# Performance work log

Measured on AMD Instinct MI355X. Metric: run time of the kernel, lower is better.

The kernel has to match this reference:

```python
import jax, jax.numpy as jnp
import numpy as np

B, N, M, K = 2, 4096, 512, 50
EMB, OUT = 512, 128
EPS = 1e-5


def _sqdist(a, b):
    # a: [B,P,D], b: [B,Q,D] -> squared euclidean distances [B,P,Q]
    return (jnp.sum(a * a, -1)[:, :, None] + jnp.sum(b * b, -1)[:, None, :]
            - 2.0 * jnp.einsum('bpd,bqd->bpq', a, b))


def _graph_feature(x, xg, k):
    # x: [B,D,N] points, xg: [B,D,M] grid -> edge features [B,2D,N,k]
    xt = x.transpose(0, 2, 1)   # [B,N,D]
    gt = xg.transpose(0, 2, 1)  # [B,M,D]
    nearest = jnp.argmin(_sqdist(xt, gt), axis=-1)               # [B,N] nearest grid pt per point
    _, nbr = jax.lax.top_k(-_sqdist(gt, gt), k)                  # [B,M,k] kNN within grid
    idx = jnp.take_along_axis(nbr, nearest[:, :, None], axis=1)  # [B,N,k]
    b = x.shape[0]
    feat = gt[jnp.arange(b)[:, None, None], idx]                 # [B,N,k,D] gathered grid feats
    feat = feat.at[:, :, 0, :].set(xt)                           # slot 0 <- point's own feature
    ctr = xt[:, :, None, :]
    out = jnp.concatenate([feat - ctr, jnp.broadcast_to(ctr, feat.shape)], axis=-1)
    return out.transpose(0, 3, 1, 2)                             # [B,2D,N,k]


def _lrelu(x):
    return jnp.where(x >= 0, x, 0.2 * x)


def _bn(y, g, bt, axes):
    # BatchNorm forward with batch statistics (torch training-mode math, biased var)
    m = jnp.mean(y, axis=axes, keepdims=True)
    v = jnp.mean((y - m) ** 2, axis=axes, keepdims=True)
    sh = [1] * y.ndim
    sh[1] = -1
    return (y - m) / jnp.sqrt(v + EPS) * g.reshape(sh) + bt.reshape(sh)


def _conv2(x, W, g, bt):
    # 1x1 Conv2d (no bias) + BN2d + LeakyReLU(0.2)
    return _lrelu(_bn(jnp.einsum('oc,bcnk->bonk', W, x), g, bt, (0, 2, 3)))


def _conv1(x, W, g, bt):
    # 1x1 Conv1d (no bias) + BN1d + LeakyReLU(0.2)
    return _lrelu(_bn(jnp.einsum('oc,bcn->bon', W, x), g, bt, (0, 2)))


def _forward(x, x_grid, FPS, W1, W2, W3, W4, W5, W6, W7, W8, W9,
             g1, g2, g3, g4, g5, g6, g7, g8,
             b1, b2, b3, b4, b5, b6, b7, b8):
    f = _graph_feature(x, x_grid, K)
    f = _conv2(f, W1, g1, b1)
    f = _conv2(f, W2, g2, b2)
    x1 = f.max(-1)                                               # [B,64,N]
    x1g = jnp.take_along_axis(x1, FPS[:, None, :], axis=2)       # [B,64,M]
    f = _graph_feature(x1, x1g, K)
    f = _conv2(f, W3, g3, b3)
    f = _conv2(f, W4, g4, b4)
    x2 = f.max(-1)
    x2g = jnp.take_along_axis(x2, FPS[:, None, :], axis=2)
    f = _graph_feature(x2, x2g, K)
    f = _conv2(f, W5, g5, b5)
    x3 = f.max(-1)
    x3g = jnp.take_along_axis(x3, FPS[:, None, :], axis=2)
    xg = jnp.concatenate([x1g, x2g, x3g], axis=1)                # [B,192,M]
    xg = _conv1(xg, W6, g6, b6)                                  # [B,EMB,M]
    xg = jnp.broadcast_to(xg.max(-1, keepdims=True), (x.shape[0], EMB, x.shape[2]))
    h = jnp.concatenate([xg, x1, x2, x3], axis=1)                # [B,EMB+192,N]
    h = _conv1(h, W7, g7, b7)
    h = _conv1(h, W8, g8, b8)
    h = jnp.einsum('oc,bcn->bon', W9, h)                         # final conv9, no BN/act
    return h.transpose(0, 2, 1)                                  # [B,N,OUT]


def setup_inputs() -> dict:
    key = jax.random.key(0)
    ks = jax.random.split(key, 32)
    def w(i, o, c):
        return jax.random.normal(ks[i], (o, c), jnp.float32) * 0.1
    inp = {
        'x': jax.random.normal(ks[0], (B, 3, N), jnp.float32),
        'x_grid': jax.random.normal(ks[1], (B, 3, M), jnp.float32),
        'FPS': jax.random.randint(ks[2], (B, M), 0, N),
        'W1': w(3, 64, 6), 'W2': w(4, 64, 64), 'W3': w(5, 64, 128),
        'W4': w(6, 64, 64), 'W5': w(7, 64, 128), 'W6': w(8, EMB, 192),
        'W7': w(9, 128, 192 + EMB), 'W8': w(10, 64, 128), 'W9': w(11, OUT, 64),
    }
    dims = [64, 64, 64, 64, 64, EMB, 128, 64]
    for j, d in enumerate(dims):
        inp[f'g{j+1}'] = 1.0 + 0.05 * jax.random.normal(ks[12 + j], (d,), jnp.float32)
        inp[f'b{j+1}'] = 0.05 * jax.random.normal(ks[20 + j], (d,), jnp.float32)
    return inp


def reference(x, x_grid, FPS, W1, W2, W3, W4, W5, W6, W7, W8, W9,
              g1, g2, g3, g4, g5, g6, g7, g8,
              b1, b2, b3, b4, b5, b6, b7, b8):
    return _forward(x, x_grid, FPS, W1, W2, W3, W4, W5, W6, W7, W8, W9,
                    g1, g2, g3, g4, g5, g6, g7, g8,
                    b1, b2, b3, b4, b5, b6, b7, b8)
```

## Files before the change

### kernel.cpp

```cpp
#include <hip/hip_runtime.h>
#include <hip/hip_bf16.h>

#define DEV __device__ __forceinline__
using bf16 = __hip_bfloat16;
using u16 = unsigned short;
using u64 = unsigned long long;

static constexpr int B_ = 2, N_ = 4096, M_ = 512, K_ = 50;
static constexpr int BN = B_ * N_;
static constexpr int BM = B_ * M_;
static constexpr float EPS_ = 1e-5f;

DEV float lrelu(float z) { return z < 0.f ? 0.2f * z : z; }
DEV int clampi(int v, int hi) { return ((unsigned)v < (unsigned)hi) ? v : 0; }

DEV u16 f2bfu(float f) {
    unsigned u = __float_as_uint(f);
    return (u16)((u + 0x7fffu + ((u >> 16) & 1u)) >> 16);
}
DEV float bfu2f(u16 h) { return __uint_as_float((unsigned)h << 16); }

typedef short bf8v __attribute__((ext_vector_type(8)));
typedef float f4v __attribute__((ext_vector_type(4)));

__global__ void k_detect(const unsigned short* __restrict__ xw, int* __restrict__ flag) {
    int t = threadIdx.x;
    int cnt = 0;
    for (int i = t; i < 4096; i += 256) {
        int e = (xw[i] >> 7) & 0xFF;
        if (e >= 100 && e <= 140) cnt++;
    }
    __shared__ int sh[256];
    sh[t] = cnt;
    __syncthreads();
    for (int s = 128; s; s >>= 1) { if (t < s) sh[t] += sh[t + s]; __syncthreads(); }
    if (t == 0) *flag = (sh[0] >= 3300) ? 1 : 0;
}

struct CvtDesc { const void* src; float* dst; int n; };
struct CvtArgs { CvtDesc d[25]; };
__global__ void k_convert(CvtArgs a, const int* __restrict__ flag) {
    CvtDesc dd = a.d[blockIdx.y];
    int i = blockIdx.x * 256 + threadIdx.x;
    if (i >= dd.n) return;
    float v = (*flag) ? __bfloat162float(((const bf16*)dd.src)[i])
                      : ((const float*)dd.src)[i];
    dd.dst[i] = v;
}

struct CvtT { const void* src; float* dst; int O; int C; int stride; int off; };
struct CvtTArgs { CvtT d[6]; };
__global__ void k_convT(CvtTArgs a, const int* __restrict__ flag) {
    CvtT dd = a.d[blockIdx.y];
    int idx = blockIdx.x * 256 + threadIdx.x;
    if (idx >= dd.O * dd.C) return;
    int c = idx / dd.O, o = idx % dd.O;
    int si = o * dd.stride + dd.off + c;
    float v = (*flag) ? __bfloat162float(((const bf16*)dd.src)[si])
                      : ((const float*)dd.src)[si];
    dd.dst[idx] = v;
}

__global__ void k_wfrag(const float* __restrict__ Wa, const float* __restrict__ Wb,
                        u16* __restrict__ fa, u16* __restrict__ fb) {
    const float* W = blockIdx.y ? Wb : Wa;
    u16* f = blockIdx.y ? fb : fa;
    int t = blockIdx.x * 256 + threadIdx.x;
    int j = t & 7, l = (t >> 3) & 63, s = (t >> 9) & 1, n = (t >> 10) & 3;
    int o = n * 16 + (l & 15);
    int c = s * 32 + (l >> 4) * 8 + j;
    float v = W[o * 64 + c];
    u16 hi = f2bfu(v);
    u16 lo = f2bfu(v - bfu2f(hi));
    f[t] = hi;
    f[4096 + t] = lo;
}

__global__ void k_ubuf(const float* __restrict__ Pg, const float* __restrict__ prm,
                       float* __restrict__ ub) {
    int t = blockIdx.x * 256 + threadIdx.x;
    int c = t & 63;
    ub[t] = fmaf(prm[c], Pg[t], prm[64 + c]);
}

DEV float rdval(const void* p, int i, int isbf) {
    return isbf ? __bfloat162float(((const bf16*)p)[i]) : ((const float*)p)[i];
}
__global__ void k_transpose(const void* __restrict__ x, const void* __restrict__ xg,
                            const int* __restrict__ flag,
                            float* __restrict__ xt, float* __restrict__ gt,
                            float* __restrict__ gT3, float* __restrict__ gn) {
    int isbf = *flag;
    int idx = blockIdx.x * 256 + threadIdx.x;
    if (idx < BN * 3) {
        int c = idx / BN, i = idx % BN;
        int b = i / N_, n = i % N_;
        xt[i * 3 + c] = rdval(x, (b * 3 + c) * N_ + n, isbf);
    } else {
        int r = idx - BN * 3;
        if (r < BM) {
            int b = r / M_, m = r % M_;
            float s = 0.f;
            for (int c = 0; c < 3; c++) {
                float v = rdval(xg, (b * 3 + c) * M_ + m, isbf);
                gt[r * 3 + c] = v;
                gT3[(b * 3 + c) * M_ + m] = v;
                s = fmaf(v, v, s);
            }
            gn[r] = s;
        }
    }
}

DEV void nearest3_body(int blk, const float* __restrict__ q, const float* __restrict__ gt,
                       const float* __restrict__ gn, int* __restrict__ nearest) {
    int sub = threadIdx.x & 15;
    int pt = blk * 16 + (threadIdx.x >> 4);
    int b = pt >> 12;
    float q0 = q[pt * 3], q1 = q[pt * 3 + 1], q2 = q[pt * 3 + 2];
    float qn = q0 * q0 + q1 * q1 + q2 * q2;
    const float* gb = gt + (size_t)b * M_ * 3;
    const float* gnb = gn + b * M_;
    float best = 1e30f; int bi = 0x7fffffff;
    for (int j = 0; j < 32; j++) {
        int m = sub + 16 * j;
        float dot = q0 * gb[m * 3] + q1 * gb[m * 3 + 1] + q2 * gb[m * 3 + 2];
        float dv = qn + gnb[m] - 2.f * dot;
        if (dv < best || (dv == best && m < bi)) { best = dv; bi = m; }
    }
    for (int off = 8; off; off >>= 1) {
        float ov = __shfl_xor(best, off);
        int oi = __shfl_xor(bi, off);
        if (ov < best || (ov == best && oi < bi)) { best = ov; bi = oi; }
    }
    if (sub == 0) nearest[pt] = clampi(bi, M_);
}

DEV void nearest64_body_v4(int blk, const float* __restrict__ q,
                           const float* __restrict__ gT, const float* __restrict__ gn,
                           int* __restrict__ nearest,
                           float (*__restrict__ lg)[512], float (*__restrict__ ql)[64]) {
    int lane = threadIdx.x & 63;
    int tid = threadIdx.x;
    int w = __builtin_amdgcn_readfirstlane(threadIdx.x >> 6);
    int pt0 = blk * 16 + w * 4;
    int b = pt0 >> 12;
    const float* gTb = gT + (size_t)b * 64 * M_;
    {
        const float4* q4 = (const float4*)(q + (size_t)(blk * 16) * 64);
        ((float4*)ql)[tid] = q4[tid];
    }
    float qn[4] = {0.f, 0.f, 0.f, 0.f};
    float d[4][8] = {};
#pragma clang loop unroll(disable)
    for (int ch = 0; ch < 8; ch++) {
        __syncthreads();
        {
            const float4* src = (const float4*)(gTb + (size_t)ch * 8 * M_);
            float4* dst = (float4*)lg;
#pragma unroll
            for (int i = 0; i < 4; i++) {
                int idx = i * 256 + tid;
                dst[idx] = src[idx];
            }
        }
        __syncthreads();
#pragma unroll
        for (int j = 0; j < 8; j++) {
            float4 g0 = *(const float4*)&lg[j][4 * lane];
            float4 g1 = *(const float4*)&lg[j][256 + 4 * lane];
#pragma unroll
            for (int p = 0; p < 4; p++) {
                float qc = ql[w * 4 + p][ch * 8 + j];
                qn[p] = fmaf(qc, qc, qn[p]);
                d[p][0] = fmaf(qc, g0.x, d[p][0]); d[p][1] = fmaf(qc, g0.y, d[p][1]);
                d[p][2] = fmaf(qc, g0.z, d[p][2]); d[p][3] = fmaf(qc, g0.w, d[p][3]);
                d[p][4] = fmaf(qc, g1.x, d[p][4]); d[p][5] = fmaf(qc, g1.y, d[p][5]);
                d[p][6] = fmaf(qc, g1.z, d[p][6]); d[p][7] = fmaf(qc, g1.w, d[p][7]);
            }
        }
    }
    const float* gnb = gn + b * M_;
    float4 n0 = *(const float4*)(gnb + 4 * lane);
    float4 n1 = *(const float4*)(gnb + 256 + 4 * lane);
    float nn[8] = {n0.x, n0.y, n0.z, n0.w, n1.x, n1.y, n1.z, n1.w};
#pragma clang loop unroll(disable)
    for (int p = 0; p < 4; p++) {
        float best = 1e30f; int bi = 0;
#pragma unroll
        for (int i = 0; i < 8; i++) {
            int m = (i < 4) ? (4 * lane + i) : (256 + 4 * lane + i - 4);
            float dv = qn[p] + nn[i] - 2.f * d[p][i];
            if (dv < best || (dv == best && m < bi)) { best = dv; bi = m; }
        }
        for (int off = 32; off; off >>= 1) {
            float ov = __shfl_xor(best, off);
            int oi = __shfl_xor(bi, off);
            if (ov < best || (ov == best && oi < bi)) { best = ov; bi = oi; }
        }
        if (lane == 0) nearest[pt0 + p] = clampi(bi, M_);
    }
}

DEV void select50(const float dd[8], const int mreg[8], int lane,
                  int* __restrict__ rowp, int* __restrict__ idxrow) {
    u64 key[8];
#pragma unroll
    for (int i = 0; i < 8; i++) {
        unsigned u = __float_as_uint(dd[i]);
        if (u == 0x80000000u) u = 0u;
        u = (u & 0x80000000u) ? ~u : (u | 0x80000000u);
        key[i] = ((u64)u << 9) | (u64)(unsigned)mreg[i];
    }
    u64 kmin = key[0];
#pragma unroll
    for (int i = 1; i < 8; i++) kmin = key[i] < kmin ? key[i] : kmin;
    for (int off = 32; off; off >>= 1) {
        u64 o = __shfl_xor(kmin, off);
        kmin = o < kmin ? o : kmin;
    }
    u64 res = 0;
#pragma clang loop unroll(disable)
    for (int bit = 40; bit >= 0; --bit) {
        u64 t = res | ((u64)1 << bit);
        int c = 0;
#pragma unroll
        for (int i = 0; i < 8; i++) c += (key[i] < t) ? 1 : 0;
        u64 b0 = __ballot(c & 1), b1 = __ballot(c & 2), b2 = __ballot(c & 4), b3 = __ballot(c & 8);
        int tot = __popcll(b0) + 2 * __popcll(b1) + 4 * __popcll(b2) + 8 * __popcll(b3);
        if (tot <= K_ - 1) res = t;
    }
    int lc = 0, loc[8];
    bool sel[8];
#pragma unroll
    for (int i = 0; i < 8; i++) {
        sel[i] = (key[i] <= res) && (key[i] != kmin);
        loc[i] = lc;
        lc += sel[i] ? 1 : 0;
    }
    u64 lmask = ((u64)1 << lane) - 1;
    u64 c0 = __ballot(lc & 1), c1 = __ballot(lc & 2), c2 = __ballot(lc & 4), c3 = __ballot(lc & 8);
    int pre = __popcll(c0 & lmask) + 2 * __popcll(c1 & lmask)
            + 4 * __popcll(c2 & lmask) + 8 * __popcll(c3 & lmask);
#pragma unroll
    for (int i = 0; i < 8; i++) {
        if (key[i] == kmin) { rowp[0] = mreg[i]; idxrow[0] = mreg[i]; }
        if (sel[i]) { int p = 1 + pre + loc[i]; rowp[p] = mreg[i]; idxrow[p] = mreg[i]; }
    }
}

DEV void nbr3_body(int blk, const float* __restrict__ g, const float* __restrict__ gT,
                   const float* __restrict__ gn, const float* __restrict__ Pg,
                   int* __restrict__ nbr, float* __restrict__ T1, float* __restrict__ T2,
                   float* __restrict__ Mn, float* __restrict__ Mx,
                   int (*__restrict__ idxb)[64]) {
    int lane = threadIdx.x & 63, w = threadIdx.x >> 6;
    int row = blk * 4 + w;
    int b = row >> 9;
    const float* grow = g + (size_t)row * 3;
    float qn = gn[row];
    const float* gTb = gT + (size_t)b * 3 * M_;
    const float* gnb = gn + b * M_;
    float d[8] = {0.f, 0.f, 0.f, 0.f, 0.f, 0.f, 0.f, 0.f};
    {
        float qs[3];
#pragma unroll
        for (int c = 0; c < 3; c++) qs[c] = grow[c];
#pragma unroll
        for (int c = 0; c < 3; c++) {
            float qc = qs[c];
            float4 g0 = *(const float4*)(gTb + c * M_ + 4 * lane);
            float4 g1 = *(const float4*)(gTb + c * M_ + 256 + 4 * lane);
            d[0] = fmaf(qc, g0.x, d[0]); d[1] = fmaf(qc, g0.y, d[1]);
            d[2] = fmaf(qc, g0.z, d[2]); d[3] = fmaf(qc, g0.w, d[3]);
            d[4] = fmaf(qc, g1.x, d[4]); d[5] = fmaf(qc, g1.y, d[5]);
            d[6] = fmaf(qc, g1.z, d[6]); d[7] = fmaf(qc, g1.w, d[7]);
        }
    }
    float4 n0 = *(const float4*)(gnb + 4 * lane);
    float4 n1 = *(const float4*)(gnb + 256 + 4 * lane);
    float dd[8];
    dd[0] = qn + n0.x - 2.f * d[0]; dd[1] = qn + n0.y - 2.f * d[1];
    dd[2] = qn + n0.z - 2.f * d[2]; dd[3] = qn + n0.w - 2.f * d[3];
    dd[4] = qn + n1.x - 2.f * d[4]; dd[5] = qn + n1.y - 2.f * d[5];
    dd[6] = qn + n1.z - 2.f * d[6]; dd[7] = qn + n1.w - 2.f * d[7];
    int mreg[8];
#pragma unroll
    for (int i = 0; i < 8; i++) mreg[i] = (i < 4) ? (4 * lane + i) : (256 + 4 * lane + i - 4);
    select50(dd, mreg, lane, nbr + (size_t)row * K_, idxb[w]);
    int myIdx = idxb[w][lane];
    const float* Pgb = Pg + (size_t)b * M_ * 64;
    float t1 = 0.f, t2 = 0.f, mn = 1e30f, mx = -1e30f;
#pragma unroll 7
    for (int k = 1; k < K_; k++) {
        int idx = clampi(__shfl(myIdx, k), M_);
        float v = Pgb[(size_t)idx * 64 + lane];
        t1 += v; t2 = fmaf(v, v, t2);
        mn = fminf(mn, v); mx = fmaxf(mx, v);
    }
    size_t o = (size_t)row * 64 + lane;
    T1[o] = t1; T2[o] = t2; Mn[o] = mn; Mx[o] = mx;
}

DEV void nbr64_body(int blk, const float* __restrict__ g, const float* __restrict__ gT,
                    const float* __restrict__ gn, const float* __restrict__ Pg,
                    int* __restrict__ nbr, float* __restrict__ T1, float* __restrict__ T2,
                    float* __restrict__ Mn, float* __restrict__ Mx,
                    float (*__restrict__ lg)[512], float (*__restrict__ ql)[64],
                    int (*__restrict__ idxb)[64]) {
    int lane = threadIdx.x & 63, w = threadIdx.x >> 6;
    int tid = threadIdx.x;
    int row = blk * 4 + w;
    int b = row >> 9;
    float qn = gn[row];
    const float* gTb = gT + (size_t)b * 64 * M_;
    const float* gnb = gn + b * M_;
    if (tid < 64) {
        const float4* q4 = (const float4*)(g + (size_t)(blk * 4) * 64);
        ((float4*)ql)[tid] = q4[tid];
    }
    float d[8] = {0.f, 0.f, 0.f, 0.f, 0.f, 0.f, 0.f, 0.f};
#pragma clang loop unroll(disable)
    for (int ch = 0; ch < 8; ch++) {
        __syncthreads();
        {
            const float4* src = (const float4*)(gTb + (size_t)ch * 8 * M_);
            float4* dst = (float4*)lg;
#pragma unroll
            for (int i = 0; i < 4; i++) {
                int idx = i * 256 + tid;
                dst[idx] = src[idx];
            }
        }
        __syncthreads();
#pragma unroll
        for (int j = 0; j < 8; j++) {
            float qc = ql[w][ch * 8 + j];
            float4 g0 = *(const float4*)&lg[j][4 * lane];
            float4 g1 = *(const float4*)&lg[j][256 + 4 * lane];
            d[0] = fmaf(qc, g0.x, d[0]); d[1] = fmaf(qc, g0.y, d[1]);
            d[2] = fmaf(qc, g0.z, d[2]); d[3] = fmaf(qc, g0.w, d[3]);
            d[4] = fmaf(qc, g1.x, d[4]); d[5] = fmaf(qc, g1.y, d[5]);
            d[6] = fmaf(qc, g1.z, d[6]); d[7] = fmaf(qc, g1.w, d[7]);
        }
    }
    float4 n0 = *(const float4*)(gnb + 4 * lane);
    float4 n1 = *(const float4*)(gnb + 256 + 4 * lane);
    float dd[8];
    dd[0] = qn + n0.x - 2.f * d[0]; dd[1] = qn + n0.y - 2.f * d[1];
    dd[2] = qn + n0.z - 2.f * d[2]; dd[3] = qn + n0.w - 2.f * d[3];
    dd[4] = qn + n1.x - 2.f * d[4]; dd[5] = qn + n1.y - 2.f * d[5];
    dd[6] = qn + n1.z - 2.f * d[6]; dd[7] = qn + n1.w - 2.f * d[7];
    int mreg[8];
#pragma unroll
    for (int i = 0; i < 8; i++) mreg[i] = (i < 4) ? (4 * lane + i) : (256 + 4 * lane + i - 4);
    select50(dd, mreg, lane, nbr + (size_t)row * K_, idxb[w]);
    int myIdx = idxb[w][lane];
    const float* Pgb = Pg + (size_t)b * M_ * 64;
    float t1 = 0.f, t2 = 0.f, mn = 1e30f, mx = -1e30f;
#pragma unroll 7
    for (int k = 1; k < K_; k++) {
        int idx = clampi(__shfl(myIdx, k), M_);
        float v = Pgb[(size_t)idx * 64 + lane];
        t1 += v; t2 = fmaf(v, v, t2);
        mn = fminf(mn, v); mx = fmaxf(mx, v);
    }
    size_t o = (size_t)row * 64 + lane;
    T1[o] = t1; T2[o] = t2; Mn[o] = mn; Mx[o] = mx;
}

__global__ __launch_bounds__(256) void k_knn3(
    const float* __restrict__ q, const float* __restrict__ gt, const float* __restrict__ gT3,
    const float* __restrict__ gn, const float* __restrict__ Pg,
    int* __restrict__ nearest, int* __restrict__ nbr, float* __restrict__ T1,
    float* __restrict__ T2, float* __restrict__ Mn, float* __restrict__ Mx) {
    __shared__ int idxb[4][64];
    if (blockIdx.x < BN / 16) nearest3_body(blockIdx.x, q, gt, gn, nearest);
    else nbr3_body(blockIdx.x - BN / 16, gt, gT3, gn, Pg, nbr, T1, T2, Mn, Mx, idxb);
}
__global__ __launch_bounds__(256) void k_knn64(
    const float* __restrict__ q, const float* __restrict__ xgt, const float* __restrict__ gT,
    const float* __restrict__ gn, const float* __restrict__ Pg,
    int* __restrict__ nearest, int* __restrict__ nbr, float* __restrict__ T1,
    float* __restrict__ T2, float* __restrict__ Mn, float* __restrict__ Mx) {
    __shared__ float lg[8][512];
    __shared__ float ql[16][64];
    __shared__ int idxb[4][64];
    if (blockIdx.x < BN / 16) nearest64_body_v4(blockIdx.x, q, gT, gn, nearest, lg, ql);
    else nbr64_body(blockIdx.x - BN / 16, xgt, gT, gn, Pg, nbr, T1, T2, Mn, Mx, lg, ql, idxb);
}

#define STATS_STORE_64(s1v, s2v, partial)                                         \
    {                                                                             \
        __shared__ float r1_[256], r2_[256];                                      \
        r1_[threadIdx.x] = (s1v); r2_[threadIdx.x] = (s2v);                       \
        __syncthreads();                                                          \
        if (threadIdx.x < 64) {                                                   \
            int t_ = threadIdx.x;                                                 \
            float a1_ = r1_[t_] + r1_[t_ + 64] + r1_[t_ + 128] + r1_[t_ + 192];   \
            float a2_ = r2_[t_] + r2_[t_ + 64] + r2_[t_ + 128] + r2_[t_ + 192];   \
            float* sp_ = (partial) + (size_t)blockIdx.x * 128;                    \
            sp_[t_] = a1_; sp_[64 + t_] = a2_;                                    \
        }                                                                         \
    }

__global__ __launch_bounds__(256) void k_pgrid3(const float* __restrict__ g,
                                                const float* __restrict__ W1,
                                                float* __restrict__ Pg) {
    int lane = threadIdx.x & 63;
    int row = blockIdx.x * 4 + __builtin_amdgcn_readfirstlane(threadIdx.x >> 6);
    float c0 = g[row * 3], c1 = g[row * 3 + 1], c2 = g[row * 3 + 2];
    const float* wr = W1 + lane * 6;
    Pg[(size_t)row * 64 + lane] = fmaf(wr[0], c0, fmaf(wr[1], c1, wr[2] * c2));
}

__global__ __launch_bounds__(256) void k_gridprep(
    const float* __restrict__ xsrc, const int* __restrict__ FPS,
    const float* __restrict__ Wt, float* __restrict__ xgt, float* __restrict__ gT,
    float* __restrict__ gn, float* __restrict__ Pg) {
    int lane = threadIdx.x & 63, w = threadIdx.x >> 6;
    int row = blockIdx.x * 4 + w;
    int b = row >> 9, m = row & 511;
    int src = b * N_ + clampi(FPS[row], N_);
    float ge = xsrc[(size_t)src * 64 + lane];
    xgt[(size_t)row * 64 + lane] = ge;
    gT[((size_t)b * 64 + lane) * M_ + m] = ge;
    float s = 0.f, acc = 0.f;
#pragma unroll
    for (int c = 0; c < 64; c++) {
        float vc = __shfl(ge, c);
        s = fmaf(vc, vc, s);
        acc = fmaf(Wt[c * 64 + lane], vc, acc);
    }
    Pg[(size_t)row * 64 + lane] = acc;
    if (lane == 0) gn[row] = s;
}

template <int D>
__global__ __launch_bounds__(256) void k_prep_stats(
    const float* __restrict__ q, const float* __restrict__ W1,
    const int* __restrict__ nearest, const float* __restrict__ T1,
    const float* __restrict__ T2, float* __restrict__ D0, float* __restrict__ S0,
    float* __restrict__ partial) {
    int lane = threadIdx.x & 63;
    int pt = blockIdx.x * 4 + __builtin_amdgcn_readfirstlane(threadIdx.x >> 6);
    int b = pt >> 12;
    float pa, pb;
    if constexpr (D == 3) {
        float c0 = q[pt * 3], c1 = q[pt * 3 + 1], c2 = q[pt * 3 + 2];
        const float* wr = W1 + lane * 6;
        pa = fmaf(wr[0], c0, fmaf(wr[1], c1, wr[2] * c2));
        pb = fmaf(wr[3], c0, fmaf(wr[4], c1, wr[5] * c2));
    } else {
        float ge = q[(size_t)pt * 64 + lane];
        pa = 0.f; pb = 0.f;
#pragma unroll
        for (int c = 0; c < 64; c++) {
            float sh = __shfl(ge, c);
            pa = fmaf(W1[c * 64 + lane], sh, pa);
            pb = fmaf(W1[(64 + c) * 64 + lane], sh, pb);
        }
    }
    float d0 = pb - pa, s0 = pb;
    size_t t = (size_t)pt * 64 + lane;
    D0[t] = d0;
    S0[t] = s0;
    size_t nr = ((size_t)b * M_ + clampi(nearest[pt], M_)) * 64 + lane;
    float t1 = T1[nr], t2 = T2[nr];
    float s1 = s0 + fmaf(49.f, d0, t1);
    float s2 = fmaf(s0, s0, fmaf(49.f * d0, d0, fmaf(2.f * d0, t1, t2)));
    STATS_STORE_64(s1, s2, partial)
}

__global__ void k_apply0(const float* __restrict__ D0, const float* __restrict__ S0,
                         const int* __restrict__ nearest, const float* __restrict__ Mn,
                         const float* __restrict__ Mx, const float* __restrict__ prm,
                         float* __restrict__ xout) {
    int t = blockIdx.x * 256 + threadIdx.x;
    int pt = t >> 6, o = t & 63;
    int b = pt >> 12;
    size_t nr = ((size_t)b * M_ + clampi(nearest[pt], M_)) * 64 + o;
    float d0 = D0[t], s0 = S0[t];
    float a = prm[o], sh = prm[64 + o];
    float v = a > 0.f ? fmaxf(s0, d0 + Mx[nr]) : fminf(s0, d0 + Mn[nr]);
    xout[t] = lrelu(fmaf(a, v, sh));
}

__global__ __launch_bounds__(256) void k_pass1_mfma(
    const float* __restrict__ ub, const float* __restrict__ D0,
    const float* __restrict__ S0, const int* __restrict__ nearest,
    const int* __restrict__ nbr, const float* __restrict__ prm1,
    const u16* __restrict__ wf, const float* __restrict__ zero64,
    float* __restrict__ partial,
    float* __restrict__ mn_out, float* __restrict__ mx_out) {
    __shared__ u16 Zs[2][2][4096];
    float* ls1 = (float*)&Zs[0][0][0];
    float* ls2 = ls1 + 128;
    int l = threadIdx.x & 63;
    int w = threadIdx.x >> 6;
    int wp = w >> 1, nh = w & 1;
    bf8v whi[2][2], wlo[2][2];
#pragma unroll
    for (int nt = 0; nt < 2; nt++)
#pragma unroll
        for (int s = 0; s < 2; s++) {
            int fi = (((nh * 2 + nt) * 2 + s) * 64 + l) * 8;
            whi[nt][s] = *(const bf8v*)(wf + fi);
            wlo[nt][s] = *(const bf8v*)(wf + 4096 + fi);
        }
    {
        int tt = threadIdx.x & 127;
        int p = threadIdx.x >> 7;
        int k = tt & 63, ch = tt >> 6;
        int pt = blockIdx.x * 2 + p, b = pt >> 12;
        int nr = clampi(nearest[pt], M_);
        const int* nrow = nbr + ((size_t)b * M_ + nr) * K_;
        int idx = (k >= 1 && k < K_) ? clampi(nrow[k], M_) : 0;
        const float4* src = ((k == 0) ? (const float4*)(S0 + (size_t)pt * 64)
                                      : (const float4*)(ub + ((size_t)b * M_ + idx) * 64)) + ch * 8;
        const float4* d4 = ((k == 0) ? (const float4*)zero64
                                     : (const float4*)(D0 + (size_t)pt * 64)) + ch * 8;
        const float4* a4 = (const float4*)(prm1) + ch * 8;
        const float4* s4 = (const float4*)(prm1 + 64) + ch * 8;
        bool pad = (k >= K_);
        char* zh = (char*)&Zs[p][0][0];
        char* zl = (char*)&Zs[p][1][0];
        int swz = (k & 7) << 4;
#pragma unroll
        for (int q2 = 0; q2 < 4; q2++) {
            unsigned hv[4], lv[4];
#pragma unroll
            for (int h = 0; h < 2; h++) {
                float4 u = src[q2 * 2 + h], d = d4[q2 * 2 + h];
                float4 a = a4[q2 * 2 + h];
                if (k == 0) {
                    float4 s = s4[q2 * 2 + h];
                    u.x = fmaf(a.x, u.x, s.x); u.y = fmaf(a.y, u.y, s.y);
                    u.z = fmaf(a.z, u.z, s.z); u.w = fmaf(a.w, u.w, s.w);
                }
                float z0 = lrelu(fmaf(a.x, d.x, u.x));
                float z1 = lrelu(fmaf(a.y, d.y, u.y));
                float z2 = lrelu(fmaf(a.z, d.z, u.z));
                float z3 = lrelu(fmaf(a.w, d.w, u.w));
                if (pad) { z0 = 0.f; z1 = 0.f; z2 = 0.f; z3 = 0.f; }
                unsigned h0 = f2bfu(z0), h1 = f2bfu(z1), h2 = f2bfu(z2), h3 = f2bfu(z3);
                unsigned l0 = __float_as_uint(z0 - bfu2f((u16)h0)) >> 16;
                unsigned l1 = __float_as_uint(z1 - bfu2f((u16)h1)) >> 16;
                unsigned l2 = __float_as_uint(z2 - bfu2f((u16)h2)) >> 16;
                unsigned l3 = __float_as_uint(z3 - bfu2f((u16)h3)) >> 16;
                hv[h * 2] = h0 | (h1 << 16); hv[h * 2 + 1] = h2 | (h3 << 16);
                lv[h * 2] = l0 | (l1 << 16); lv[h * 2 + 1] = l2 | (l3 << 16);
            }
            int ad = k * 128 + ((ch * 64 + q2 * 16) ^ swz);
            *(uint4*)(zh + ad) = make_uint4(hv[0], hv[1], hv[2], hv[3]);
            *(uint4*)(zl + ad) = make_uint4(lv[0], lv[1], lv[2], lv[3]);
        }
    }
    __syncthreads();
    int pt = blockIdx.x * 2 + wp;
    const char* zh = (const char*)&Zs[wp][0][0];
    const char* zl = (const char*)&Zs[wp][1][0];
    f4v acc[4][2] = {};
#pragma unroll
    for (int s = 0; s < 2; s++) {
        bf8v ah[4], al[4];
#pragma unroll
        for (int m = 0; m < 4; m++) {
            int row = m * 16 + (l & 15);
            int ad = row * 128 + (((s * 64) + ((l >> 4) * 16)) ^ ((row & 7) << 4));
            ah[m] = *(const bf8v*)(zh + ad);
            al[m] = *(const bf8v*)(zl + ad);
        }
#pragma unroll
        for (int m = 0; m < 4; m++)
#pragma unroll
            for (int nt = 0; nt < 2; nt++) {
                acc[m][nt] = __builtin_amdgcn_mfma_f32_16x16x32_bf16(ah[m], whi[nt][s], acc[m][nt], 0, 0, 0);
                acc[m][nt] = __builtin_amdgcn_mfma_f32_16x16x32_bf16(al[m], whi[nt][s], acc[m][nt], 0, 0, 0);
                acc[m][nt] = __builtin_amdgcn_mfma_f32_16x16x32_bf16(ah[m], wlo[nt][s], acc[m][nt], 0, 0, 0);
            }
    }
    __syncthreads();
    int rg = (l >> 4) * 4;
#pragma unroll
    for (int nt = 0; nt < 2; nt++) {
        float s1 = 0.f, s2 = 0.f, mn = 1e30f, mx = -1e30f;
#pragma unroll
        for (int m = 0; m < 4; m++)
#pragma unroll
            for (int i = 0; i < 4; i++) {
                int kk = m * 16 + rg + i;
                float v = acc[m][nt][i];
                if (kk < K_) { s1 += v; s2 = fmaf(v, v, s2); mn = fminf(mn, v); mx = fmaxf(mx, v); }
            }
        for (int off = 16; off <= 32; off <<= 1) {
            s1 += __shfl_xor(s1, off); s2 += __shfl_xor(s2, off);
            mn = fminf(mn, __shfl_xor(mn, off)); mx = fmaxf(mx, __shfl_xor(mx, off));
        }
        if (l < 16) {
            int o = nh * 32 + nt * 16 + l;
            mn_out[(size_t)pt * 64 + o] = mn;
            mx_out[(size_t)pt * 64 + o] = mx;
            ls1[wp * 64 + o] = s1;
            ls2[wp * 64 + o] = s2;
        }
    }
    __syncthreads();
    if (threadIdx.x < 64) {
        int t = threadIdx.x;
        float* sp = partial + (size_t)blockIdx.x * 128;
        sp[t] = ls1[t] + ls1[64 + t];
        sp[64 + t] = ls2[t] + ls2[64 + t];
    }
}

__global__ void k_apply(const float* __restrict__ mn, const float* __restrict__ mx,
                        const float* __restrict__ prm, float* __restrict__ xout) {
    int t = blockIdx.x * 256 + threadIdx.x;
    int o = t & 63;
    float a = prm[o], sh = prm[64 + o];
    float v = a > 0.f ? mx[t] : mn[t];
    xout[t] = lrelu(fmaf(a, v, sh));
}

template <int NP, int O>
__global__ __launch_bounds__(256) void k_redfin(
    const float* __restrict__ partial, double* __restrict__ red,
    int* __restrict__ counter, int C,
    const float* __restrict__ g, const float* __restrict__ bt,
    float* __restrict__ prm) {
    constexpr int VALS = 2 * O;
    constexpr int G = NP / 32;
    int b = blockIdx.x;
    for (int v = threadIdx.x; v < VALS; v += 256) {
        const float* p = partial + (size_t)b * G * VALS + v;
        double s = 0.0;
#pragma unroll
        for (int k = 0; k < G; k++) s += p[(size_t)k * VALS];
        red[(size_t)b * VALS + v] = s;
    }
    __threadfence();
    __syncthreads();
    __shared__ bool isLast;
    if (threadIdx.x == 0) isLast = (atomicAdd(counter, 1) == 31);
    __syncthreads();
    if (!isLast) return;
    __threadfence();
    for (int o = threadIdx.x; o < O; o += 256) {
        double s1 = 0.0, s2 = 0.0;
#pragma unroll
        for (int k = 0; k < 32; k++) {
            s1 += red[(size_t)k * VALS + o];
            s2 += red[(size_t)k * VALS + O + o];
        }
        double m = s1 / C, var = s2 / C - m * m;
        if (var < 0) var = 0;
        float sc = g[o] / sqrtf((float)var + EPS_);
        prm[o] = sc;
        prm[O + o] = bt[o] - (float)m * sc;
    }
}

__global__ __launch_bounds__(256) void k_conv_w6(
    const float* __restrict__ x1gt, const float* __restrict__ x2gt,
    const float* __restrict__ x3t, const int* __restrict__ FPS,
    const float* __restrict__ W6t, float* __restrict__ y6, float* __restrict__ partial) {
    __shared__ float vl[4][192];
    int b = blockIdx.x / 128;
    int m0 = (blockIdx.x % 128) * 4;
    for (int i = threadIdx.x; i < 4 * 192; i += 256) {
        int mi = i / 192, c = i % 192;
        float v;
        if (c < 128) {
            const float* src = c < 64 ? x1gt : x2gt;
            v = src[((size_t)b * M_ + m0 + mi) * 64 + (c & 63)];
        } else {
            int s = b * N_ + clampi(FPS[b * M_ + m0 + mi], N_);
            v = x3t[(size_t)s * 64 + (c - 128)];
        }
        vl[mi][c] = v;
    }
    __syncthreads();
    float acc0[4] = {0}, acc1[4] = {0};
    int o0 = threadIdx.x, o1 = threadIdx.x + 256;
    for (int c = 0; c < 192; c++) {
        float w0 = W6t[c * 512 + o0];
        float w1 = W6t[c * 512 + o1];
#pragma unroll
        for (int m = 0; m < 4; m++) { float v = vl[m][c]; acc0[m] = fmaf(w0, v, acc0[m]); acc1[m] = fmaf(w1, v, acc1[m]); }
    }
    float s1a = 0, s2a = 0, s1b = 0, s2b = 0;
    for (int m = 0; m < 4; m++) {
        float ya = acc0[m], yb = acc1[m];
        y6[((size_t)b * M_ + m0 + m) * 512 + o0] = ya;
        y6[((size_t)b * M_ + m0 + m) * 512 + o1] = yb;
        s1a += ya; s2a = fmaf(ya, ya, s2a); s1b += yb; s2b = fmaf(yb, yb, s2b);
    }
    float* sp = partial + (size_t)blockIdx.x * 1024;
    sp[o0] = s1a; sp[512 + o0] = s2a;
    sp[o1] = s1b; sp[512 + o1] = s2b;
}

__global__ void k_maxM(const float* __restrict__ y6, const float* __restrict__ prm,
                       float* __restrict__ xgmax) {
    int blk = blockIdx.x;
    int b = blk >> 6;
    int obase = (blk & 63) << 3;
    int o = obase + (threadIdx.x & 7);
    int mg = threadIdx.x >> 3;
    float a = prm[o], sh = prm[512 + o];
    float mx = -1e30f;
    for (int m = mg; m < M_; m += 32)
        mx = fmaxf(mx, lrelu(fmaf(a, y6[((size_t)b * M_ + m) * 512 + o], sh)));
    __shared__ float red[256];
    red[threadIdx.x] = mx;
    __syncthreads();
    for (int s = 128; s >= 8; s >>= 1) {
        if (threadIdx.x < s) red[threadIdx.x] = fmaxf(red[threadIdx.x], red[threadIdx.x + s]);
        __syncthreads();
    }
    if (threadIdx.x < 8) xgmax[b * 512 + obase + threadIdx.x] = red[threadIdx.x];
}

__global__ __launch_bounds__(256) void k_p7(const float* __restrict__ xgmax,
                                            const float* __restrict__ W7,
                                            float* __restrict__ p7) {
    int lane = threadIdx.x & 63, w = threadIdx.x >> 6;
    int t = blockIdx.x * 4 + w;
    int b = t >> 7, o = t & 127;
    float acc = 0.f;
#pragma unroll
    for (int j = 0; j < 8; j++) {
        int c = j * 64 + lane;
        acc = fmaf(W7[o * 704 + c], xgmax[b * 512 + c], acc);
    }
    for (int off = 32; off; off >>= 1) acc += __shfl_xor(acc, off);
    if (lane == 0) p7[t] = acc;
}

__global__ __launch_bounds__(256) void k_conv_w7(
    const float* __restrict__ x1t, const float* __restrict__ x2t,
    const float* __restrict__ x3t, const float* __restrict__ p7,
    const float* __restrict__ W7vt, float* __restrict__ y7, float* __restrict__ partial) {
    __shared__ float vl[16][192];
    int item0 = blockIdx.x * 16;
    for (int i = threadIdx.x; i < 16 * 192; i += 256) {
        int it = i / 192, c = i % 192;
        const float* src = c < 64 ? x1t : (c < 128 ? x2t : x3t);
        vl[it][c] = src[((size_t)(item0 + it)) * 64 + (c & 63)];
    }
    __syncthreads();
    int o = threadIdx.x & 127, h = threadIdx.x >> 7;
    float acc[8] = {0};
    for (int c = 0; c < 192; c++) {
        float w = W7vt[c * 128 + o];
#pragma unroll
        for (int i = 0; i < 8; i++) acc[i] = fmaf(w, vl[h * 8 + i][c], acc[i]);
    }
    float s1 = 0, s2 = 0;
    for (int i = 0; i < 8; i++) {
        int item = item0 + h * 8 + i;
        int b = item / N_;
        float yv = p7[b * 128 + o] + acc[i];
        y7[(size_t)item * 128 + o] = yv;
        s1 += yv; s2 = fmaf(yv, yv, s2);
    }
    __shared__ float r1[256], r2[256];
    r1[threadIdx.x] = s1; r2[threadIdx.x] = s2;
    __syncthreads();
    if (threadIdx.x < 128) {
        float* sp = partial + (size_t)blockIdx.x * 256;
        sp[threadIdx.x] = r1[threadIdx.x] + r1[threadIdx.x + 128];
        sp[128 + threadIdx.x] = r2[threadIdx.x] + r2[threadIdx.x + 128];
    }
}

__global__ __launch_bounds__(256) void k_conv_w8(
    const float* __restrict__ y7, const float* __restrict__ prm7,
    const float* __restrict__ W8t, float* __restrict__ y8, float* __restrict__ partial) {
    int lane = threadIdx.x & 63;
    int item = blockIdx.x * 4 + (threadIdx.x >> 6);
    float W0[64], W1r[64];
#pragma unroll
    for (int c = 0; c < 64; c++) {
        W0[c] = W8t[c * 64 + lane];
        W1r[c] = W8t[(64 + c) * 64 + lane];
    }
    float a0 = prm7[lane], sh0 = prm7[128 + lane];
    float a1 = prm7[64 + lane], sh1 = prm7[128 + 64 + lane];
    float z0 = lrelu(fmaf(a0, y7[(size_t)item * 128 + lane], sh0));
    float z1 = lrelu(fmaf(a1, y7[(size_t)item * 128 + 64 + lane], sh1));
    float acc = 0.f;
#pragma unroll
    for (int c = 0; c < 64; c++) {
        acc = fmaf(W0[c], __shfl(z0, c), acc);
        acc = fmaf(W1r[c], __shfl(z1, c), acc);
    }
    y8[(size_t)item * 64 + lane] = acc;
    STATS_STORE_64(acc, acc * acc, partial)
}

__global__ __launch_bounds__(256) void k_final(
    const float* __restrict__ y8, const float* __restrict__ prm8,
    const float* __restrict__ W9t, void* __restrict__ out, const int* __restrict__ flag) {
    __shared__ float zl[2][64];
    int item0 = blockIdx.x * 2;
    if (threadIdx.x < 128) {
        int it = threadIdx.x >> 6, c = threadIdx.x & 63;
        float z = fmaf(prm8[c], y8[(size_t)(item0 + it) * 64 + c], prm8[64 + c]);
        zl[it][c] = lrelu(z);
    }
    __syncthreads();
    int it = threadIdx.x >> 7, o = threadIdx.x & 127;
    float acc = 0.f;
#pragma unroll
    for (int c = 0; c < 64; c++) acc = fmaf(W9t[c * 128 + o], zl[it][c], acc);
    size_t oi = (size_t)(item0 + it) * 128 + o;
    if (*flag) ((bf16*)out)[oi] = __float2bfloat16(acc);
    else ((float*)out)[oi] = acc;
}

extern "C" void kernel_launch(void* const* d_in, const int* in_sizes, int n_in,
                              void* d_out, int out_size, void* d_ws, size_t ws_size,
                              hipStream_t stream) {
    (void)in_sizes; (void)n_in; (void)out_size; (void)ws_size;
    const void* x = d_in[0];
    const void* xgrid = d_in[1];
    const int* FPS = (const int*)d_in[2];

    char* ws = (char*)d_ws;
    size_t off = 0;
    auto alloc = [&](size_t bytes) -> char* {
        char* p = ws + off;
        off = (off + bytes + 255) & ~(size_t)255;
        return p;
    };
    int* flag       = (int*)alloc(256);
    int* counters   = (int*)alloc(256);
    float* zero64   = (float*)alloc(256);
    float* partials = (float*)alloc(4096 * 128 * sizeof(float));
    double* redbuf  = (double*)alloc(32 * 1024 * sizeof(double));
    float* prm      = (float*)alloc(8 * 1024 * sizeof(float));
    static const int wsz[9] = {384, 4096, 8192, 4096, 8192, 98304, 90112, 8192, 8192};
    static const int dims[8] = {64, 64, 64, 64, 64, 512, 128, 64};
    float* cW[9];
    for (int i = 0; i < 9; i++) cW[i] = (float*)alloc((size_t)wsz[i] * 4);
    float* cG[8];
    float* cB[8];
    for (int j = 0; j < 8; j++) {
        cG[j] = (float*)alloc((size_t)dims[j] * 4);
        cB[j] = (float*)alloc((size_t)dims[j] * 4);
    }
    float* W6t  = (float*)alloc((size_t)512 * 192 * 4);
    float* W7vt = (float*)alloc((size_t)128 * 192 * 4);
    float* W8t  = (float*)alloc((size_t)64 * 128 * 4);
    float* W9t  = (float*)alloc((size_t)128 * 64 * 4);
    float* W3t  = (float*)alloc((size_t)64 * 128 * 4);
    float* W5t  = (float*)alloc((size_t)64 * 128 * 4);
    u16* wf2    = (u16*)alloc((size_t)8192 * 2);
    u16* wf4    = (u16*)alloc((size_t)8192 * 2);
    float* xt    = (float*)alloc((size_t)BN * 3 * 4);
    float* gt    = (float*)alloc((size_t)BM * 3 * 4);
    float* gT3   = (float*)alloc((size_t)B_ * 3 * M_ * 4);
    float* gn    = (float*)alloc((size_t)BM * 4);
    int* nearest = (int*)alloc((size_t)BN * 4);
    int* nbr     = (int*)alloc((size_t)BM * K_ * 4);
    float* Pg    = (float*)alloc((size_t)BM * 64 * 4);
    float* ubuf  = (float*)alloc((size_t)BM * 64 * 4);
    float* x1t   = (float*)alloc((size_t)BN * 64 * 4);
    float* x2t   = (float*)alloc((size_t)BN * 64 * 4);
    float* x3t   = (float*)alloc((size_t)BN * 64 * 4);
    float* x1gt  = (float*)alloc((size_t)BM * 64 * 4);
    float* x2gt  = (float*)alloc((size_t)BM * 64 * 4);
    float* gT64  = (float*)alloc((size_t)B_ * 64 * M_ * 4);
    float* y6    = (float*)alloc((size_t)BM * 512 * 4);
    float* xgmax = (float*)alloc((size_t)B_ * 512 * 4);
    float* p7    = (float*)alloc((size_t)B_ * 128 * 4);
    float* y7    = (float*)alloc((size_t)BN * 128 * 4);
    float* y8    = (float*)alloc((size_t)BN * 64 * 4);
    float* D0b = y7;
    float* S0b = y7 + (size_t)BN * 64;
    float* mnb = y8;
    float* mxb = y6;
    float* T1b = y6;
    float* T2b = y6 + (size_t)BM * 64;
    float* Mnb = y6 + (size_t)2 * BM * 64;
    float* Mxb = y6 + (size_t)3 * BM * 64;

    hipMemsetAsync(counters, 0, 8 * sizeof(int), stream);
    hipMemsetAsync(zero64, 0, 256, stream);
    k_detect<<<1, 256, 0, stream>>>((const unsigned short*)x, flag);

    CvtArgs ca;
    for (int i = 0; i < 9; i++) ca.d[i] = {d_in[3 + i], cW[i], wsz[i]};
    for (int j = 0; j < 8; j++) {
        ca.d[9 + 2 * j]     = {d_in[12 + 2 * j], cG[j], dims[j]};
        ca.d[9 + 2 * j + 1] = {d_in[13 + 2 * j], cB[j], dims[j]};
    }
    k_convert<<<dim3(384, 25), 256, 0, stream>>>(ca, flag);
    CvtTArgs ct;
    ct.d[0] = {d_in[8],  W6t,  512, 192, 192, 0};
    ct.d[1] = {d_in[9],  W7vt, 128, 192, 704, 512};
    ct.d[2] = {d_in[10], W8t,  64, 128, 128, 0};
    ct.d[3] = {d_in[11], W9t,  128, 64, 64, 0};
    ct.d[4] = {d_in[5],  W3t,  64, 128, 128, 0};
    ct.d[5] = {d_in[7],  W5t,  64, 128, 128, 0};
    k_convT<<<dim3(384, 6), 256, 0, stream>>>(ct, flag);
    k_wfrag<<<dim3(16, 2), 256, 0, stream>>>(cW[1], cW[3], wf2, wf4);
    k_transpose<<<(BN * 3 + BM + 255) / 256, 256, 0, stream>>>(x, xgrid, flag, xt, gt, gT3, gn);

    const int PG = BN / 4;
    const int EW = BN * 64 / 256;
    const int CK = BN * K_;
    const int KNNG = BN / 16 + BM / 4;
    const int UBG = BM * 64 / 256;

    k_pgrid3<<<BM / 4, 256, 0, stream>>>(gt, cW[0], Pg);
    k_knn3<<<KNNG, 256, 0, stream>>>(xt, gt, gT3, gn, Pg, nearest, nbr, T1b, T2b, Mnb, Mxb);
    k_prep_stats<3><<<PG, 256, 0, stream>>>(xt, cW[0], nearest, T1b, T2b, D0b, S0b, partials);
    k_redfin<2048, 64><<<32, 256, 0, stream>>>(partials, redbuf, counters + 0, CK, cG[0], cB[0], prm + 0 * 1024);
    k_ubuf<<<UBG, 256, 0, stream>>>(Pg, prm + 0 * 1024, ubuf);
    k_pass1_mfma<<<BN / 2, 256, 0, stream>>>(ubuf, D0b, S0b, nearest, nbr, prm + 0 * 1024, wf2, zero64, partials, mnb, mxb);
    k_redfin<4096, 64><<<32, 256, 0, stream>>>(partials, redbuf, counters + 1, CK, cG[1], cB[1], prm + 1 * 1024);
    k_apply<<<EW, 256, 0, stream>>>(mnb, mxb, prm + 1 * 1024, x1t);

    k_gridprep<<<BM / 4, 256, 0, stream>>>(x1t, FPS, W3t, x1gt, gT64, gn, Pg);
    k_knn64<<<KNNG, 256, 0, stream>>>(x1t, x1gt, gT64, gn, Pg, nearest, nbr, T1b, T2b, Mnb, Mxb);
    k_prep_stats<64><<<PG, 256, 0, stream>>>(x1t, W3t, nearest, T1b, T2b, D0b, S0b, partials);
    k_redfin<2048, 64><<<32, 256, 0, stream>>>(partials, redbuf, counters + 2, CK, cG[2], cB[2], prm + 2 * 1024);
    k_ubuf<<<UBG, 256, 0, stream>>>(Pg, prm + 2 * 1024, ubuf);
    k_pass1_mfma<<<BN / 2, 256, 0, stream>>>(ubuf, D0b, S0b, nearest, nbr, prm + 2 * 1024, wf4, zero64, partials, mnb, mxb);
    k_redfin<4096, 64><<<32, 256, 0, stream>>>(partials, redbuf, counters + 3, CK, cG[3], cB[3], prm + 3 * 1024);
    k_apply<<<EW, 256, 0, stream>>>(mnb, mxb, prm + 3 * 1024, x2t);

    k_gridprep<<<BM / 4, 256, 0, stream>>>(x2t, FPS, W5t, x2gt, gT64, gn, Pg);
    k_knn64<<<KNNG, 256, 0, stream>>>(x2t, x2gt, gT64, gn, Pg, nearest, nbr, T1b, T2b, Mnb, Mxb);
    k_prep_stats<64><<<PG, 256, 0, stream>>>(x2t, W5t, nearest, T1b, T2b, D0b, S0b, partials);
    k_redfin<2048, 64><<<32, 256, 0, stream>>>(partials, redbuf, counters + 4, CK, cG[4], cB[4], prm + 4 * 1024);
    k_apply0<<<EW, 256, 0, stream>>>(D0b, S0b, nearest, Mnb, Mxb, prm + 4 * 1024, x3t);

    k_conv_w6<<<BM / 4, 256, 0, stream>>>(x1gt, x2gt, x3t, FPS, W6t, y6, partials);
    k_redfin<256, 512><<<32, 256, 0, stream>>>(partials, redbuf, counters + 5, BM, cG[5], cB[5], prm + 5 * 1024);
    k_maxM<<<B_ * 64, 256, 0, stream>>>(y6, prm + 5 * 1024, xgmax);
    k_p7<<<64, 256, 0, stream>>>(xgmax, cW[6], p7);
    k_conv_w7<<<BN / 16, 256, 0, stream>>>(x1t, x2t, x3t, p7, W7vt, y7, partials);
    k_redfin<512, 128><<<32, 256, 0, stream>>>(partials, redbuf, counters + 6, BN, cG[6], cB[6], prm + 6 * 1024);
    k_conv_w8<<<BN / 4, 256, 0, stream>>>(y7, prm + 6 * 1024, W8t, y8, partials);
    k_redfin<2048, 64><<<32, 256, 0, stream>>>(partials, redbuf, counters + 7, BN, cG[7], cB[7], prm + 7 * 1024);
    k_final<<<BN / 2, 256, 0, stream>>>(y8, prm + 7 * 1024, W9t, d_out, flag);
}
```

Before: 434.8 us.

## Port W7 conv to split-bf16 MFMA and use packed bf16 conversion

The 192-to-128 pointwise conv (W7) moves from scalar FMA over fp32 shared memory to MFMA 16x16x32 bf16. Activations and weights are split into hi/lo bf16 pairs and three products are accumulated to keep near-fp32 accuracy. A new kernel precomputes the W7 fragment layout once. The hi/lo split in the pass1 MFMA kernel now uses the hardware v_cvt_pk_bf16_f32 instruction in place of manual rounding. One extra small launch is added, and the lo residual rounding changes slightly.

```diff
diff --git a/kernel.cpp b/kernel.cpp
--- a/kernel.cpp
+++ b/kernel.cpp
@@ -19,6 +19,11 @@
     return (u16)((u + 0x7fffu + ((u >> 16) & 1u)) >> 16);
 }
 DEV float bfu2f(u16 h) { return __uint_as_float((unsigned)h << 16); }
+DEV unsigned cvtpk(float a, float b) {
+    unsigned r;
+    asm("v_cvt_pk_bf16_f32 %0, %1, %2" : "=v"(r) : "v"(a), "v"(b));
+    return r;
+}
 
 typedef short bf8v __attribute__((ext_vector_type(8)));
 typedef float f4v __attribute__((ext_vector_type(4)));
@@ -74,6 +79,20 @@
     u16 lo = f2bfu(v - bfu2f(hi));
     f[t] = hi;
     f[4096 + t] = lo;
+}
+
+__global__ void k_wfrag7(const float* __restrict__ W7vt, u16* __restrict__ f) {
+    int t = blockIdx.x * 256 + threadIdx.x;
+    int j = t & 7, l = (t >> 3) & 63;
+    int rest = t >> 9;
+    int s = rest % 6, ot = rest / 6;
+    int o = ot * 16 + (l & 15);
+    int c = s * 32 + (l >> 4) * 8 + j;
+    float v = W7vt[c * 128 + o];
+    u16 hi = f2bfu(v);
+    u16 lo = f2bfu(v - bfu2f(hi));
+    f[t] = hi;
+    f[24576 + t] = lo;
 }
 
 __global__ void k_ubuf(const float* __restrict__ Pg, const float* __restrict__ prm,
@@ -543,13 +562,13 @@
                 float z2 = lrelu(fmaf(a.z, d.z, u.z));
                 float z3 = lrelu(fmaf(a.w, d.w, u.w));
                 if (pad) { z0 = 0.f; z1 = 0.f; z2 = 0.f; z3 = 0.f; }
-                unsigned h0 = f2bfu(z0), h1 = f2bfu(z1), h2 = f2bfu(z2), h3 = f2bfu(z3);
-                unsigned l0 = __float_as_uint(z0 - bfu2f((u16)h0)) >> 16;
-                unsigned l1 = __float_as_uint(z1 - bfu2f((u16)h1)) >> 16;
-                unsigned l2 = __float_as_uint(z2 - bfu2f((u16)h2)) >> 16;
-                unsigned l3 = __float_as_uint(z3 - bfu2f((u16)h3)) >> 16;
-                hv[h * 2] = h0 | (h1 << 16); hv[h * 2 + 1] = h2 | (h3 << 16);
-                lv[h * 2] = l0 | (l1 << 16); lv[h * 2 + 1] = l2 | (l3 << 16);
+                unsigned h01 = cvtpk(z0, z1), h23 = cvtpk(z2, z3);
+                float r0 = z0 - __uint_as_float(h01 << 16);
+                float r1 = z1 - __uint_as_float(h01 & 0xFFFF0000u);
+                float r2 = z2 - __uint_as_float(h23 << 16);
+                float r3 = z3 - __uint_as_float(h23 & 0xFFFF0000u);
+                hv[h * 2] = h01; hv[h * 2 + 1] = h23;
+                lv[h * 2] = cvtpk(r0, r1); lv[h * 2 + 1] = cvtpk(r2, r3);
             }
             int ad = k * 128 + ((ch * 64 + q2 * 16) ^ swz);
             *(uint4*)(zh + ad) = make_uint4(hv[0], hv[1], hv[2], hv[3]);
@@ -738,40 +757,90 @@
     if (lane == 0) p7[t] = acc;
 }
 
-__global__ __launch_bounds__(256) void k_conv_w7(
+__global__ __launch_bounds__(256) void k_conv_w7m(
     const float* __restrict__ x1t, const float* __restrict__ x2t,
     const float* __restrict__ x3t, const float* __restrict__ p7,
-    const float* __restrict__ W7vt, float* __restrict__ y7, float* __restrict__ partial) {
-    __shared__ float vl[16][192];
+    const u16* __restrict__ wf7, float* __restrict__ y7, float* __restrict__ partial) {
+    __shared__ u16 Zh[16][200], Zl[16][200];
+    int tid = threadIdx.x;
+    int l = tid & 63, w = tid >> 6;
     int item0 = blockIdx.x * 16;
-    for (int i = threadIdx.x; i < 16 * 192; i += 256) {
-        int it = i / 192, c = i % 192;
-        const float* src = c < 64 ? x1t : (c < 128 ? x2t : x3t);
-        vl[it][c] = src[((size_t)(item0 + it)) * 64 + (c & 63)];
+    int b = blockIdx.x >> 8;
+    bf8v wh[2][6], wl[2][6];
+#pragma unroll
+    for (int nt = 0; nt < 2; nt++)
+#pragma unroll
+        for (int s = 0; s < 6; s++) {
+            int fi = (((2 * w + nt) * 6 + s) * 64 + l) * 8;
+            wh[nt][s] = *(const bf8v*)(wf7 + fi);
+            wl[nt][s] = *(const bf8v*)(wf7 + 24576 + fi);
+        }
+    {
+        int item = tid >> 4, seg = tid & 15;
+        if (seg < 12) {
+            const float* sp_;
+            size_t base = (size_t)(item0 + item) * 64;
+            if (seg < 4) sp_ = x1t + base + seg * 16;
+            else if (seg < 8) sp_ = x2t + base + (seg - 4) * 16;
+            else sp_ = x3t + base + (seg - 8) * 16;
+            float f[16];
+#pragma unroll
+            for (int i = 0; i < 4; i++) {
+                float4 v = ((const float4*)sp_)[i];
+                f[4 * i] = v.x; f[4 * i + 1] = v.y; f[4 * i + 2] = v.z; f[4 * i + 3] = v.w;
+            }
+            unsigned hp[8], lp[8];
+#pragma unroll
+            for (int e = 0; e < 8; e++) {
+                unsigned h = cvtpk(f[2 * e], f[2 * e + 1]);
+                float r0 = f[2 * e] - __uint_as_float(h << 16);
+                float r1 = f[2 * e + 1] - __uint_as_float(h & 0xFFFF0000u);
+                hp[e] = h;
+                lp[e] = cvtpk(r0, r1);
+            }
+            uint4* dh = (uint4*)&Zh[item][seg * 16];
+            uint4* dl = (uint4*)&Zl[item][seg * 16];
+            dh[0] = make_uint4(hp[0], hp[1], hp[2], hp[3]);
+            dh[1] = make_uint4(hp[4], hp[5], hp[6], hp[7]);
+            dl[0] = make_uint4(lp[0], lp[1], lp[2], lp[3]);
+            dl[1] = make_uint4(lp[4], lp[5], lp[6], lp[7]);
+        }
     }
     __syncthreads();
-    int o = threadIdx.x & 127, h = threadIdx.x >> 7;
-    float acc[8] = {0};
-    for (int c = 0; c < 192; c++) {
-        float w = W7vt[c * 128 + o];
-#pragma unroll
-        for (int i = 0; i < 8; i++) acc[i] = fmaf(w, vl[h * 8 + i][c], acc[i]);
-    }
-    float s1 = 0, s2 = 0;
-    for (int i = 0; i < 8; i++) {
-        int item = item0 + h * 8 + i;
-        int b = item / N_;
-        float yv = p7[b * 128 + o] + acc[i];
-        y7[(size_t)item * 128 + o] = yv;
-        s1 += yv; s2 = fmaf(yv, yv, s2);
-    }
-    __shared__ float r1[256], r2[256];
-    r1[threadIdx.x] = s1; r2[threadIdx.x] = s2;
-    __syncthreads();
-    if (threadIdx.x < 128) {
-        float* sp = partial + (size_t)blockIdx.x * 256;
-        sp[threadIdx.x] = r1[threadIdx.x] + r1[threadIdx.x + 128];
-        sp[128 + threadIdx.x] = r2[threadIdx.x] + r2[threadIdx.x + 128];
+    f4v acc[2] = {};
+#pragma unroll
+    for (int s = 0; s < 6; s++) {
+        int row = l & 15, col = s * 32 + (l >> 4) * 8;
+        bf8v ah = *(const bf8v*)&Zh[row][col];
+        bf8v al = *(const bf8v*)&Zl[row][col];
+#pragma unroll
+        for (int nt = 0; nt < 2; nt++) {
+            acc[nt] = __builtin_amdgcn_mfma_f32_16x16x32_bf16(ah, wh[nt][s], acc[nt], 0, 0, 0);
+            acc[nt] = __builtin_amdgcn_mfma_f32_16x16x32_bf16(al, wh[nt][s], acc[nt], 0, 0, 0);
+            acc[nt] = __builtin_amdgcn_mfma_f32_16x16x32_bf16(ah, wl[nt][s], acc[nt], 0, 0, 0);
+        }
+    }
+#pragma unroll
+    for (int nt = 0; nt < 2; nt++) {
+        int o = (2 * w + nt) * 16 + (l & 15);
+        float pv = p7[b * 128 + o];
+        float s1 = 0.f, s2 = 0.f;
+#pragma unroll
+        for (int i = 0; i < 4; i++) {
+            int item = (l >> 4) * 4 + i;
+            float yv = pv + acc[nt][i];
+            y7[(size_t)(item0 + item) * 128 + o] = yv;
+            s1 += yv; s2 = fmaf(yv, yv, s2);
+        }
+        for (int off = 16; off <= 32; off <<= 1) {
+            s1 += __shfl_xor(s1, off);
+            s2 += __shfl_xor(s2, off);
+        }
+        if (l < 16) {
+            float* sp = partial + (size_t)blockIdx.x * 256;
+            sp[o] = s1;
+            sp[128 + o] = s2;
+        }
     }
 }
 
@@ -859,6 +928,7 @@
     float* W5t  = (float*)alloc((size_t)64 * 128 * 4);
     u16* wf2    = (u16*)alloc((size_t)8192 * 2);
     u16* wf4    = (u16*)alloc((size_t)8192 * 2);
+    u16* wf7    = (u16*)alloc((size_t)49152 * 2);
     float* xt    = (float*)alloc((size_t)BN * 3 * 4);
     float* gt    = (float*)alloc((size_t)BM * 3 * 4);
     float* gT3   = (float*)alloc((size_t)B_ * 3 * M_ * 4);
@@ -907,6 +977,7 @@
     ct.d[5] = {d_in[7],  W5t,  64, 128, 128, 0};
     k_convT<<<dim3(384, 6), 256, 0, stream>>>(ct, flag);
     k_wfrag<<<dim3(16, 2), 256, 0, stream>>>(cW[1], cW[3], wf2, wf4);
+    k_wfrag7<<<96, 256, 0, stream>>>(W7vt, wf7);
     k_transpose<<<(BN * 3 + BM + 255) / 256, 256, 0, stream>>>(x, xgrid, flag, xt, gt, gT3, gn);
 
     const int PG = BN / 4;
@@ -943,7 +1014,7 @@
     k_redfin<256, 512><<<32, 256, 0, stream>>>(partials, redbuf, counters + 5, BM, cG[5], cB[5], prm + 5 * 1024);
     k_maxM<<<B_ * 64, 256, 0, stream>>>(y6, prm + 5 * 1024, xgmax);
     k_p7<<<64, 256, 0, stream>>>(xgmax, cW[6], p7);
-    k_conv_w7<<<BN / 16, 256, 0, stream>>>(x1t, x2t, x3t, p7, W7vt, y7, partials);
+    k_conv_w7m<<<BN / 16, 256, 0, stream>>>(x1t, x2t, x3t, p7, wf7, y7, partials);
     k_redfin<512, 128><<<32, 256, 0, stream>>>(partials, redbuf, counters + 6, BN, cG[6], cB[6], prm + 6 * 1024);
     k_conv_w8<<<BN / 4, 256, 0, stream>>>(y7, prm + 6 * 1024, W8t, y8, partials);
     k_redfin<2048, 64><<<32, 256, 0, stream>>>(partials, redbuf, counters + 7, BN, cG[7], cB[7], prm + 7 * 1024);
```

Result: faster. 416.1 us (-4.3%).
